# Kernel tuning notes

Hardware: AMD Instinct MI355X
Metric: run time of the kernel (lower is better)

## Reference

```python
import jax, jax.numpy as jnp
import numpy as np

LN_EPS = 1e-5      # torch nn.LayerNorm default
NORM_EPS = 1e-12   # torch F.normalize default


def _layer_norm(x, gamma, beta):
    mu = jnp.mean(x, axis=-1, keepdims=True)
    var = jnp.mean((x - mu) ** 2, axis=-1, keepdims=True)
    return (x - mu) * jax.lax.rsqrt(var + LN_EPS) * gamma + beta


def _l2_normalize_rows(w):
    n = jnp.sqrt(jnp.sum(w * w, axis=1, keepdims=True))
    return w / jnp.maximum(n, NORM_EPS)


def setup_inputs() -> dict:
    key = jax.random.key(0)
    B, D = 32768, 512
    ks = jax.random.split(key, 4)
    return {
        "stimulus": jax.random.normal(ks[0], (B, D), dtype=jnp.float32),
        "prev_activation": jax.random.normal(ks[1], (B, D), dtype=jnp.float32),
        "W": jax.random.normal(ks[2], (D, D), dtype=jnp.float32),
        "Wr": jax.random.normal(ks[3], (D, D), dtype=jnp.float32),
        "alpha": jnp.full((D,), 0.1, dtype=jnp.float32),
        "decay": jnp.full((D,), 0.01, dtype=jnp.float32),
        "ln_act_gamma": jnp.ones((D,), dtype=jnp.float32),
        "ln_act_beta": jnp.zeros((D,), dtype=jnp.float32),
        "ln_rec_gamma": jnp.ones((D,), dtype=jnp.float32),
        "ln_rec_beta": jnp.zeros((D,), dtype=jnp.float32),
    }


def reference(stimulus, prev_activation, W, Wr, alpha, decay,
              ln_act_gamma, ln_act_beta, ln_rec_gamma, ln_rec_beta):
    # recurrent path
    rec_out = prev_activation @ Wr                      # [B, D]
    rec_norm = _layer_norm(rec_out, ln_rec_gamma, ln_rec_beta)
    # stimulus path
    stim_out = stimulus @ W                             # [B, D]
    final = jax.nn.relu(stim_out + rec_norm)
    final = _layer_norm(final, ln_act_gamma, ln_act_beta)

    # Hebbian weight update (detached in the original module)
    heb_upd = jnp.einsum('bi,bj->ij', stimulus, stim_out) * alpha[None, :]
    rec_upd = jnp.einsum('bi,bj->ij', prev_activation, rec_out) * alpha[None, :]
    # diag(decay) @ W is a row-wise broadcast scale
    new_W = _l2_normalize_rows(W + heb_upd - decay[:, None] * W)
    new_Wr = _l2_normalize_rows(Wr + rec_upd - decay[:, None] * Wr)

    return final, new_W, new_Wr
```

## Files before the change

### kernel.cpp

```cpp
#include <hip/hip_runtime.h>
#include <stdint.h>

typedef unsigned int u32;
typedef unsigned short u16;
typedef float  f32x4 __attribute__((ext_vector_type(4)));
typedef u32    u32x4 __attribute__((ext_vector_type(4)));
typedef __bf16 bf16x8 __attribute__((ext_vector_type(8)));

static __device__ __forceinline__ u16 f2bf(float f){
  u32 u = __builtin_bit_cast(u32, f);
  return (u16)((u + 0x7FFFu + ((u >> 16) & 1u)) >> 16);
}

static __device__ __forceinline__ void async16(const void* g, void* l){
  __builtin_amdgcn_global_load_lds((const __attribute__((address_space(1))) u32*)g,
                                   (__attribute__((address_space(3))) u32*)l, 16, 0, 0);
}

static __device__ __forceinline__ float wave_sum(float v){
#pragma unroll
  for (int o = 32; o > 0; o >>= 1) v += __shfl_xor(v, o, 64);
  return v;
}

static __device__ __forceinline__ void prep_tcvt(int sid, const float* __restrict__ W,
                                                 const float* __restrict__ Wr,
                                                 u16* __restrict__ Wt, u16* __restrict__ Wrt,
                                                 u16* lt){
  const int tix = sid & 7, tiy = (sid >> 3) & 7, tiz = sid >> 6;
  const float* __restrict__ src = tiz ? Wr : W;
  u16* __restrict__ dst = tiz ? Wrt : Wt;
  const int c0 = tix * 64, r0 = tiy * 64;
  const int tid = threadIdx.x;
  const int rr = tid >> 4, c4 = tid & 15;
#pragma unroll
  for (int p = 0; p < 4; ++p){
    int r = rr + p*16;
    f32x4 f = *(const f32x4*)(src + (size_t)(r0 + r)*512 + c0 + c4*4);
#pragma unroll
    for (int e = 0; e < 4; ++e) lt[(c4*4 + e)*72 + r] = f2bf(f[e]);
  }
  __syncthreads();
  const int c = tid >> 2, bg = tid & 3;
  const u32x4* lp = (const u32x4*)(lt + c*72 + bg*16);
  u32x4 w0 = lp[0], w1 = lp[1];
  u16* drow = dst + (size_t)(c0 + c)*512 + r0 + bg*16;
  *(u32x4*)drow = w0;
  *(u32x4*)(drow + 8) = w1;
}

__global__ __launch_bounds__(256) void k_prep2(const float* __restrict__ S, const float* __restrict__ P,
                                               const float* __restrict__ W, const float* __restrict__ Wr,
                                               u16* __restrict__ SN, u16* __restrict__ PN,
                                               u16* __restrict__ Wt, u16* __restrict__ Wrt){
  __shared__ u16 lt[64*72];
  const int id = blockIdx.x;
  if (id < 2048){
    const int mat = id >> 10, sub = id & 1023;
    const float* __restrict__ src = mat ? P : S;
    u16* __restrict__ dst = mat ? PN : SN;
    const size_t o0 = ((size_t)sub*256 + threadIdx.x) * 8;
#pragma unroll
    for (int j = 0; j < 8; ++j){
      size_t o = o0 + (size_t)j*2097152;
      f32x4 a = *(const f32x4*)(src + o);
      f32x4 b = *(const f32x4*)(src + o + 4);
      u32x4 w;
      w[0] = (u32)f2bf(a[0]) | ((u32)f2bf(a[1]) << 16);
      w[1] = (u32)f2bf(a[2]) | ((u32)f2bf(a[3]) << 16);
      w[2] = (u32)f2bf(b[0]) | ((u32)f2bf(b[1]) << 16);
      w[3] = (u32)f2bf(b[2]) | ((u32)f2bf(b[3]) << 16);
      *(u32x4*)(dst + o) = w;
    }
  } else {
    prep_tcvt(id - 2048, W, Wr, Wt, Wrt, lt);
  }
}

__global__ __launch_bounds__(512) void k_gemm_fwd(const u16* __restrict__ SN, const u16* __restrict__ PN,
                                                  const u16* __restrict__ Wt, const u16* __restrict__ Wrt,
                                                  u16* __restrict__ SO, u16* __restrict__ RO,
                                                  u16* __restrict__ SOT, u16* __restrict__ ROT){
  __shared__ char smem[67584];
  u16* sA = (u16*)smem;
  u16* sB = (u16*)(smem + 32768);
  const int tid = threadIdx.x;
  const int lane = tid & 63, wid = tid >> 6;
  const int wm = wid >> 1, wn = wid & 1;
  const int l15 = lane & 15, q = lane >> 4;
  const int id = blockIdx.x;
  const int c8 = id & 7, g = id >> 3;
  const int sel = g >> 6, h = g & 63;
  const int yb = c8*16 + (h >> 2), xb = h & 3;
  const int m0 = yb * 256, n0 = xb * 128;
  const u16* __restrict__ A  = sel ? PN  : SN;
  const u16* __restrict__ Bt = sel ? Wrt : Wt;
  u16* __restrict__ Cn = sel ? RO  : SO;
  u16* __restrict__ Ct = sel ? ROT : SOT;

  f32x4 acc[4][4];
  const f32x4 vzero = {0.f, 0.f, 0.f, 0.f};
#pragma unroll
  for (int a = 0; a < 4; ++a)
#pragma unroll
    for (int b = 0; b < 4; ++b) acc[a][b] = vzero;

#pragma unroll 1
  for (int kt = 0; kt < 8; ++kt){
    const int k0 = kt*64;
#pragma unroll
    for (int it = 0; it < 4; ++it){
      int gg0 = it*512 + tid;
      int r = gg0 >> 3, gp = gg0 & 7, gsw = gp ^ (r & 7);
      async16(A + (size_t)(m0 + r)*512 + k0 + gsw*8, (char*)sA + (size_t)gg0*16);
    }
#pragma unroll
    for (int it = 0; it < 2; ++it){
      int gg0 = it*512 + tid;
      int r = gg0 >> 3, gp = gg0 & 7, gsw = gp ^ (r & 7);
      async16(Bt + (size_t)(n0 + r)*512 + k0 + gsw*8, (char*)sB + (size_t)gg0*16);
    }
    __syncthreads();
#pragma unroll
    for (int kk = 0; kk < 2; ++kk){
      bf16x8 af[4], bfv[4];
#pragma unroll
      for (int mt = 0; mt < 4; ++mt){
        int r = wm*64 + mt*16 + l15;
        int gsw = (kk*4 + q) ^ (r & 7);
        af[mt] = *(const bf16x8*)(sA + (size_t)(r*8 + gsw)*8);
      }
#pragma unroll
      for (int nt = 0; nt < 4; ++nt){
        int r = wn*64 + nt*16 + l15;
        int gsw = (kk*4 + q) ^ (r & 7);
        bfv[nt] = *(const bf16x8*)(sB + (size_t)(r*8 + gsw)*8);
      }
#pragma unroll
      for (int mt = 0; mt < 4; ++mt)
#pragma unroll
        for (int nt = 0; nt < 4; ++nt)
          acc[mt][nt] = __builtin_amdgcn_mfma_f32_16x16x32_bf16(af[mt], bfv[nt], acc[mt][nt], 0, 0, 0);
    }
    __syncthreads();
  }

  u16* lt = (u16*)smem;
#pragma unroll
  for (int mt = 0; mt < 4; ++mt)
#pragma unroll
    for (int nt = 0; nt < 4; ++nt){
      f32x4 v = acc[mt][nt];
      u16 b0 = f2bf(v[0]), b1 = f2bf(v[1]), b2 = f2bf(v[2]), b3 = f2bf(v[3]);
      int n = wn*64 + nt*16 + l15;
      int mb = wm*64 + mt*16 + q*4;
      u16* cn = Cn + (size_t)(m0 + mb)*512 + n0 + n;
      cn[0] = b0; cn[512] = b1; cn[1024] = b2; cn[1536] = b3;
      *(u32*)(lt + n*264 + mb)     = (u32)b0 | ((u32)b1 << 16);
      *(u32*)(lt + n*264 + mb + 2) = (u32)b2 | ((u32)b3 << 16);
    }
  __syncthreads();
#pragma unroll
  for (int p = 0; p < 8; ++p){
    int gg0 = p*512 + tid;
    int n = gg0 >> 5, mg = gg0 & 31;
    u32x4 w = *(const u32x4*)(lt + n*264 + mg*8);
    *(u32x4*)(Ct + (size_t)(n0 + n)*32768 + m0 + mg*8) = w;
  }
}

__global__ __launch_bounds__(512) void k_gemm_upd(const u16* __restrict__ A0, const u16* __restrict__ B0,
                                                  const u16* __restrict__ A1, const u16* __restrict__ B1,
                                                  float* __restrict__ part){
  __shared__ char smem[67584];
  char* sAn = smem;
  u32*  sAt = (u32*)(smem + 16384);
  u16*  sB  = (u16*)(smem + 34816);
  const int tid = threadIdx.x;
  const int lane = tid & 63, wid = tid >> 6;
  const int wm = wid >> 2, wn = wid & 3;
  const int l15 = lane & 15, q = lane >> 4;
  const int id = blockIdx.x;
  const int c8 = id & 7, g = id >> 3;
  const int zz = c8*8 + (g >> 3);
  const int xy = g & 7;
  const int mat = zz >> 5, sp = zz & 31;
  const int yb = xy & 3, xb = xy >> 2;
  const u16* __restrict__ A = mat ? A1 : A0;
  const u16* __restrict__ B = mat ? B1 : B0;
  const int m0 = yb * 128, n0 = xb * 256;
  const int kb = sp * 1024;
  const int base_c = tid >> 5, pr = tid & 31;
  const int ce = (base_c + pr) & 15;

  f32x4 acc[4][4];
  const f32x4 vzero = {0.f, 0.f, 0.f, 0.f};
#pragma unroll
  for (int a = 0; a < 4; ++a)
#pragma unroll
    for (int b = 0; b < 4; ++b) acc[a][b] = vzero;

#pragma unroll 1
  for (int kt = 0; kt < 16; ++kt){
    const int k0 = kb + kt*64;
#pragma unroll
    for (int it = 0; it < 2; ++it){
      int gg0 = it*512 + tid;
      int r = gg0 >> 4, gp = gg0 & 15;
      async16(A + (size_t)(k0 + r)*512 + m0 + gp*8, sAn + (size_t)gg0*16);
    }
#pragma unroll
    for (int it = 0; it < 4; ++it){
      int gg0 = it*512 + tid;
      int r = gg0 >> 3, gp = gg0 & 7, gsw = gp ^ (r & 7);
      async16(B + (size_t)(n0 + r)*32768 + k0 + gsw*8, (char*)sB + (size_t)gg0*16);
    }
    __syncthreads();
    {
      u32x4 r0 = *(const u32x4*)(sAn + (size_t)(2*pr)*256 + ce*16);
      u32x4 r1 = *(const u32x4*)(sAn + (size_t)(2*pr)*256 + 256 + ce*16);
#pragma unroll
      for (int e = 0; e < 4; ++e){
        u32 lo = r0[e], hi = r1[e];
        sAt[(ce*8 + 2*e    )*36 + pr] = (lo & 0xFFFFu) | (hi << 16);
        sAt[(ce*8 + 2*e + 1)*36 + pr] = (lo >> 16) | (hi & 0xFFFF0000u);
      }
    }
    __syncthreads();
#pragma unroll
    for (int kk = 0; kk < 2; ++kk){
      bf16x8 af[4], bfv[4];
#pragma unroll
      for (int mt = 0; mt < 4; ++mt){
        int r = wm*64 + mt*16 + l15;
        af[mt] = *(const bf16x8*)(sAt + (size_t)r*36 + kk*16 + q*4);
      }
#pragma unroll
      for (int nt = 0; nt < 4; ++nt){
        int r = wn*64 + nt*16 + l15;
        int gsw = (kk*4 + q) ^ (r & 7);
        bfv[nt] = *(const bf16x8*)(sB + (size_t)(r*8 + gsw)*8);
      }
#pragma unroll
      for (int mt = 0; mt < 4; ++mt)
#pragma unroll
        for (int nt = 0; nt < 4; ++nt)
          acc[mt][nt] = __builtin_amdgcn_mfma_f32_16x16x32_bf16(af[mt], bfv[nt], acc[mt][nt], 0, 0, 0);
    }
    __syncthreads();
  }

  float* dst = part + (size_t)(mat*32 + sp)*262144;
#pragma unroll
  for (int mt = 0; mt < 4; ++mt)
#pragma unroll
    for (int nt = 0; nt < 4; ++nt){
      f32x4 v = acc[mt][nt];
      int n = wn*64 + nt*16 + l15;
      int mb = wm*64 + mt*16 + q*4;
      float* d = dst + (size_t)(m0 + mb)*512 + n0 + n;
      d[0] = v[0]; d[512] = v[1]; d[1024] = v[2]; d[1536] = v[3];
    }
}

__global__ __launch_bounds__(256) void k_ln(const u16* __restrict__ SO, const u16* __restrict__ RO,
                                            const float* __restrict__ ga, const float* __restrict__ ba,
                                            const float* __restrict__ gr, const float* __restrict__ br,
                                            float* __restrict__ out){
  const int wid = threadIdx.x >> 6, lane = threadIdx.x & 63;
  const size_t b = (size_t)blockIdx.x*4 + wid;
  const int c = lane*8;
  float x[8], t[8];
  {
    u32x4 u = *(const u32x4*)(RO + b*512 + c);
#pragma unroll
    for (int i = 0; i < 4; ++i){
      u32 w = u[i];
      x[2*i]   = __uint_as_float(w << 16);
      x[2*i+1] = __uint_as_float(w & 0xFFFF0000u);
    }
  }
  float s = 0.f, ss = 0.f;
#pragma unroll
  for (int e = 0; e < 8; ++e){ s += x[e]; ss += x[e]*x[e]; }
  s = wave_sum(s); ss = wave_sum(ss);
  float mu = s*(1.f/512.f);
  float var = fmaxf(ss*(1.f/512.f) - mu*mu, 0.f);
  float rs = rsqrtf(var + 1e-5f);
  f32x4 g0 = *(const f32x4*)(gr + c), g1 = *(const f32x4*)(gr + c + 4);
  f32x4 h0 = *(const f32x4*)(br + c), h1 = *(const f32x4*)(br + c + 4);
  {
    u32x4 u = *(const u32x4*)(SO + b*512 + c);
    float so[8];
#pragma unroll
    for (int i = 0; i < 4; ++i){
      u32 w = u[i];
      so[2*i]   = __uint_as_float(w << 16);
      so[2*i+1] = __uint_as_float(w & 0xFFFF0000u);
    }
#pragma unroll
    for (int e = 0; e < 4; ++e) t[e]   = fmaxf(so[e]   + (x[e]  -mu)*rs*g0[e] + h0[e], 0.f);
#pragma unroll
    for (int e = 0; e < 4; ++e) t[4+e] = fmaxf(so[4+e] + (x[4+e]-mu)*rs*g1[e] + h1[e], 0.f);
  }
  float s2 = 0.f, ss2 = 0.f;
#pragma unroll
  for (int e = 0; e < 8; ++e){ s2 += t[e]; ss2 += t[e]*t[e]; }
  s2 = wave_sum(s2); ss2 = wave_sum(ss2);
  float mu2 = s2*(1.f/512.f);
  float var2 = fmaxf(ss2*(1.f/512.f) - mu2*mu2, 0.f);
  float rs2 = rsqrtf(var2 + 1e-5f);
  f32x4 G0 = *(const f32x4*)(ga + c), G1 = *(const f32x4*)(ga + c + 4);
  f32x4 H0 = *(const f32x4*)(ba + c), H1 = *(const f32x4*)(ba + c + 4);
  f32x4 o0, o1;
#pragma unroll
  for (int e = 0; e < 4; ++e){
    o0[e] = (t[e]   - mu2)*rs2*G0[e] + H0[e];
    o1[e] = (t[4+e] - mu2)*rs2*G1[e] + H1[e];
  }
  *(f32x4*)(out + b*512 + c)     = o0;
  *(f32x4*)(out + b*512 + c + 4) = o1;
}

__global__ __launch_bounds__(256) void k_finalize(const float* __restrict__ W0, const float* __restrict__ W1,
                                                  const float* __restrict__ part,
                                                  const float* __restrict__ alpha, const float* __restrict__ decay,
                                                  float* __restrict__ out){
  const int i = blockIdx.x, mat = blockIdx.y;
  const int t = threadIdx.x;
  const float* Wm = mat ? W1 : W0;
  const float* pb = part + (size_t)mat*32*262144 + (size_t)i*512;
  const float dc = decay[i];
  float v[2], ssq = 0.f;
#pragma unroll
  for (int h = 0; h < 2; ++h){
    int j = t + h*256;
    float acc = 0.f;
#pragma unroll
    for (int sp = 0; sp < 32; ++sp) acc += pb[(size_t)sp*262144 + j];
    float val = Wm[(size_t)i*512 + j]*(1.f - dc) + alpha[j]*acc;
    v[h] = val; ssq += val*val;
  }
  float wsum = wave_sum(ssq);
  __shared__ float red[4];
  const int lane = t & 63, wid = t >> 6;
  if (lane == 0) red[wid] = wsum;
  __syncthreads();
  float tot = red[0] + red[1] + red[2] + red[3];
  float rn = 1.f / fmaxf(sqrtf(tot), 1e-12f);
  out[(size_t)mat*262144 + (size_t)i*512 + t]       = v[0]*rn;
  out[(size_t)mat*262144 + (size_t)i*512 + t + 256] = v[1]*rn;
}

extern "C" void kernel_launch(void* const* d_in, const int* in_sizes, int n_in,
                              void* d_out, int out_size, void* d_ws, size_t ws_size,
                              hipStream_t stream) {
  const float* S  = (const float*)d_in[0];
  const float* P  = (const float*)d_in[1];
  const float* W  = (const float*)d_in[2];
  const float* Wr = (const float*)d_in[3];
  const float* alpha = (const float*)d_in[4];
  const float* decay = (const float*)d_in[5];
  const float* ga = (const float*)d_in[6];
  const float* ba = (const float*)d_in[7];
  const float* gr = (const float*)d_in[8];
  const float* br = (const float*)d_in[9];
  float* out = (float*)d_out;

  char* ws = (char*)d_ws;
  u16* SN  = (u16*)(ws);
  u16* PN  = (u16*)(ws + 33554432);
  u16* SOT = (u16*)(ws + 67108864);
  u16* ROT = (u16*)(ws + 100663296);
  u16* SO  = (u16*)(ws + 134217728);
  u16* RO  = (u16*)(ws + 167772160);
  u16* Wt  = (u16*)(ws + 201326592);
  u16* Wrt = (u16*)(ws + 201850880);
  float* part = (float*)(ws + 134217728);

  k_prep2<<<dim3(2176), dim3(256), 0, stream>>>(S, P, W, Wr, SN, PN, Wt, Wrt);
  k_gemm_fwd<<<dim3(1024), dim3(512), 0, stream>>>(SN, PN, Wt, Wrt, SO, RO, SOT, ROT);
  k_ln<<<dim3(8192), dim3(256), 0, stream>>>(SO, RO, ga, ba, gr, br, out);
  k_gemm_upd<<<dim3(512), dim3(512), 0, stream>>>(SN, SOT, PN, ROT, part);
  k_finalize<<<dim3(512, 2), dim3(256), 0, stream>>>(W, Wr, part, alpha, decay, out + 16777216);
}
```

Baseline: 325.5 us.

## Fuse forward GEMMs with both LayerNorms into one full-row kernel

Replaces the separate forward GEMM and LayerNorm kernels with one kernel in which each block computes full 512-column rows for both the stimulus and recurrent GEMMs, keeps the stimulus result packed in registers, and applies both LayerNorms in-register using a cross-wave shared-memory reduction. This drops the SO/RO row-major bf16 intermediates and the extra LN pass over them, still writing only the transposed copies needed by the update GEMM. The prep kernel is also reshaped to one chunk per block. The catch is that only 256 blocks are launched, each carrying a large register accumulator, so occupancy and parallelism drop.

```diff
diff --git a/kernel.cpp b/kernel.cpp
--- a/kernel.cpp
+++ b/kernel.cpp
@@ -23,107 +23,75 @@
   return v;
 }
 
-static __device__ __forceinline__ void prep_tcvt(int sid, const float* __restrict__ W,
-                                                 const float* __restrict__ Wr,
-                                                 u16* __restrict__ Wt, u16* __restrict__ Wrt,
-                                                 u16* lt){
-  const int tix = sid & 7, tiy = (sid >> 3) & 7, tiz = sid >> 6;
-  const float* __restrict__ src = tiz ? Wr : W;
-  u16* __restrict__ dst = tiz ? Wrt : Wt;
-  const int c0 = tix * 64, r0 = tiy * 64;
-  const int tid = threadIdx.x;
-  const int rr = tid >> 4, c4 = tid & 15;
-#pragma unroll
-  for (int p = 0; p < 4; ++p){
-    int r = rr + p*16;
-    f32x4 f = *(const f32x4*)(src + (size_t)(r0 + r)*512 + c0 + c4*4);
-#pragma unroll
-    for (int e = 0; e < 4; ++e) lt[(c4*4 + e)*72 + r] = f2bf(f[e]);
-  }
-  __syncthreads();
-  const int c = tid >> 2, bg = tid & 3;
-  const u32x4* lp = (const u32x4*)(lt + c*72 + bg*16);
-  u32x4 w0 = lp[0], w1 = lp[1];
-  u16* drow = dst + (size_t)(c0 + c)*512 + r0 + bg*16;
-  *(u32x4*)drow = w0;
-  *(u32x4*)(drow + 8) = w1;
-}
-
-__global__ __launch_bounds__(256) void k_prep2(const float* __restrict__ S, const float* __restrict__ P,
-                                               const float* __restrict__ W, const float* __restrict__ Wr,
-                                               u16* __restrict__ SN, u16* __restrict__ PN,
-                                               u16* __restrict__ Wt, u16* __restrict__ Wrt){
+__global__ __launch_bounds__(256) void k_prep(const float* __restrict__ S, const float* __restrict__ P,
+                                              const float* __restrict__ W, const float* __restrict__ Wr,
+                                              u16* __restrict__ SN, u16* __restrict__ PN,
+                                              u16* __restrict__ Wt, u16* __restrict__ Wrt){
   __shared__ u16 lt[64*72];
   const int id = blockIdx.x;
-  if (id < 2048){
-    const int mat = id >> 10, sub = id & 1023;
-    const float* __restrict__ src = mat ? P : S;
-    u16* __restrict__ dst = mat ? PN : SN;
-    const size_t o0 = ((size_t)sub*256 + threadIdx.x) * 8;
-#pragma unroll
-    for (int j = 0; j < 8; ++j){
-      size_t o = o0 + (size_t)j*2097152;
-      f32x4 a = *(const f32x4*)(src + o);
-      f32x4 b = *(const f32x4*)(src + o + 4);
-      u32x4 w;
-      w[0] = (u32)f2bf(a[0]) | ((u32)f2bf(a[1]) << 16);
-      w[1] = (u32)f2bf(a[2]) | ((u32)f2bf(a[3]) << 16);
-      w[2] = (u32)f2bf(b[0]) | ((u32)f2bf(b[1]) << 16);
-      w[3] = (u32)f2bf(b[2]) | ((u32)f2bf(b[3]) << 16);
-      *(u32x4*)(dst + o) = w;
-    }
+  if (id < 16384){
+    const int y = id >> 13, x = id & 8191;
+    const float* __restrict__ src = y ? P : S;
+    u16* __restrict__ dst = y ? PN : SN;
+    size_t i = ((size_t)x*256 + threadIdx.x) * 8;
+    f32x4 a = *(const f32x4*)(src + i);
+    f32x4 b = *(const f32x4*)(src + i + 4);
+    u32x4 w;
+    w[0] = (u32)f2bf(a[0]) | ((u32)f2bf(a[1]) << 16);
+    w[1] = (u32)f2bf(a[2]) | ((u32)f2bf(a[3]) << 16);
+    w[2] = (u32)f2bf(b[0]) | ((u32)f2bf(b[1]) << 16);
+    w[3] = (u32)f2bf(b[2]) | ((u32)f2bf(b[3]) << 16);
+    *(u32x4*)(dst + i) = w;
   } else {
-    prep_tcvt(id - 2048, W, Wr, Wt, Wrt, lt);
-  }
-}
-
-__global__ __launch_bounds__(512) void k_gemm_fwd(const u16* __restrict__ SN, const u16* __restrict__ PN,
-                                                  const u16* __restrict__ Wt, const u16* __restrict__ Wrt,
-                                                  u16* __restrict__ SO, u16* __restrict__ RO,
-                                                  u16* __restrict__ SOT, u16* __restrict__ ROT){
-  __shared__ char smem[67584];
+    const int sid = id - 16384;
+    const int tix = sid & 7, tiy = (sid >> 3) & 7, tiz = sid >> 6;
+    const float* __restrict__ src = tiz ? Wr : W;
+    u16* __restrict__ dst = tiz ? Wrt : Wt;
+    const int c0 = tix * 64, r0 = tiy * 64;
+    const int tid = threadIdx.x;
+    const int rr = tid >> 4, c4 = tid & 15;
+#pragma unroll
+    for (int p = 0; p < 4; ++p){
+      int r = rr + p*16;
+      f32x4 f = *(const f32x4*)(src + (size_t)(r0 + r)*512 + c0 + c4*4);
+#pragma unroll
+      for (int e = 0; e < 4; ++e) lt[(c4*4 + e)*72 + r] = f2bf(f[e]);
+    }
+    __syncthreads();
+    const int c = tid >> 2, bg = tid & 3;
+    const u32x4* lp = (const u32x4*)(lt + c*72 + bg*16);
+    u32x4 w0 = lp[0], w1 = lp[1];
+    u16* drow = dst + (size_t)(c0 + c)*512 + r0 + bg*16;
+    *(u32x4*)drow = w0;
+    *(u32x4*)(drow + 8) = w1;
+  }
+}
+
+
+static __device__ __forceinline__ void gemm_phase(const u16* __restrict__ A, const u16* __restrict__ Bt,
+                                                  f32x4 (&acc)[4][8], char* smem,
+                                                  int tid, int wm, int wn, int l15, int q, int m0){
   u16* sA = (u16*)smem;
-  u16* sB = (u16*)(smem + 32768);
-  const int tid = threadIdx.x;
-  const int lane = tid & 63, wid = tid >> 6;
-  const int wm = wid >> 1, wn = wid & 1;
-  const int l15 = lane & 15, q = lane >> 4;
-  const int id = blockIdx.x;
-  const int c8 = id & 7, g = id >> 3;
-  const int sel = g >> 6, h = g & 63;
-  const int yb = c8*16 + (h >> 2), xb = h & 3;
-  const int m0 = yb * 256, n0 = xb * 128;
-  const u16* __restrict__ A  = sel ? PN  : SN;
-  const u16* __restrict__ Bt = sel ? Wrt : Wt;
-  u16* __restrict__ Cn = sel ? RO  : SO;
-  u16* __restrict__ Ct = sel ? ROT : SOT;
-
-  f32x4 acc[4][4];
-  const f32x4 vzero = {0.f, 0.f, 0.f, 0.f};
-#pragma unroll
-  for (int a = 0; a < 4; ++a)
-#pragma unroll
-    for (int b = 0; b < 4; ++b) acc[a][b] = vzero;
-
+  u16* sB = (u16*)(smem + 16384);
 #pragma unroll 1
   for (int kt = 0; kt < 8; ++kt){
     const int k0 = kt*64;
 #pragma unroll
-    for (int it = 0; it < 4; ++it){
-      int gg0 = it*512 + tid;
-      int r = gg0 >> 3, gp = gg0 & 7, gsw = gp ^ (r & 7);
-      async16(A + (size_t)(m0 + r)*512 + k0 + gsw*8, (char*)sA + (size_t)gg0*16);
-    }
-#pragma unroll
     for (int it = 0; it < 2; ++it){
-      int gg0 = it*512 + tid;
-      int r = gg0 >> 3, gp = gg0 & 7, gsw = gp ^ (r & 7);
-      async16(Bt + (size_t)(n0 + r)*512 + k0 + gsw*8, (char*)sB + (size_t)gg0*16);
+      int gg = it*512 + tid;
+      int r = gg >> 3, gp = gg & 7, gsw = gp ^ (r & 7);
+      async16(A + (size_t)(m0 + r)*512 + k0 + gsw*8, (char*)sA + (size_t)gg*16);
+    }
+#pragma unroll
+    for (int it = 0; it < 8; ++it){
+      int gg = it*512 + tid;
+      int r = gg >> 3, gp = gg & 7, gsw = gp ^ (r & 7);
+      async16(Bt + (size_t)r*512 + k0 + gsw*8, (char*)sB + (size_t)gg*16);
     }
     __syncthreads();
 #pragma unroll
     for (int kk = 0; kk < 2; ++kk){
-      bf16x8 af[4], bfv[4];
+      bf16x8 af[4], bfv[8];
 #pragma unroll
       for (int mt = 0; mt < 4; ++mt){
         int r = wm*64 + mt*16 + l15;
@@ -131,42 +99,204 @@
         af[mt] = *(const bf16x8*)(sA + (size_t)(r*8 + gsw)*8);
       }
 #pragma unroll
-      for (int nt = 0; nt < 4; ++nt){
-        int r = wn*64 + nt*16 + l15;
+      for (int nt = 0; nt < 8; ++nt){
+        int r = wn*128 + nt*16 + l15;
         int gsw = (kk*4 + q) ^ (r & 7);
         bfv[nt] = *(const bf16x8*)(sB + (size_t)(r*8 + gsw)*8);
       }
 #pragma unroll
       for (int mt = 0; mt < 4; ++mt)
 #pragma unroll
-        for (int nt = 0; nt < 4; ++nt)
+        for (int nt = 0; nt < 8; ++nt)
           acc[mt][nt] = __builtin_amdgcn_mfma_f32_16x16x32_bf16(af[mt], bfv[nt], acc[mt][nt], 0, 0, 0);
     }
     __syncthreads();
   }
-
+}
+
+static __device__ __forceinline__ void store_T(const f32x4 (&acc)[4][8], u16* __restrict__ Ct, char* smem,
+                                               int tid, int wm, int wn, int l15, int q, int m0){
   u16* lt = (u16*)smem;
+#pragma unroll 1
+  for (int jc = 0; jc < 4; ++jc){
+    if (wn == jc){
+#pragma unroll
+      for (int mt = 0; mt < 4; ++mt)
+#pragma unroll
+        for (int nt = 0; nt < 8; ++nt){
+          f32x4 v = acc[mt][nt];
+          int jl = nt*16 + l15;
+          int bl = wm*64 + mt*16 + q*4;
+          *(u32*)(lt + jl*264 + bl)     = (u32)f2bf(v[0]) | ((u32)f2bf(v[1]) << 16);
+          *(u32*)(lt + jl*264 + bl + 2) = (u32)f2bf(v[2]) | ((u32)f2bf(v[3]) << 16);
+        }
+    }
+    __syncthreads();
+#pragma unroll
+    for (int p = 0; p < 4; ++p){
+      int gg = p*512 + tid;
+      int j = gg >> 4, mg = gg & 15;
+      u32x4 w = *(const u32x4*)(lt + j*264 + mg*8);
+      *(u32x4*)(Ct + (size_t)(jc*128 + j)*32768 + m0 + mg*8) = w;
+    }
+    __syncthreads();
+  }
+}
+
+__global__ __launch_bounds__(512) void k_fused(const u16* __restrict__ SN, const u16* __restrict__ PN,
+                                               const u16* __restrict__ Wt, const u16* __restrict__ Wrt,
+                                               const float* __restrict__ ga, const float* __restrict__ ba,
+                                               const float* __restrict__ gr, const float* __restrict__ br,
+                                               u16* __restrict__ SOT, u16* __restrict__ ROT,
+                                               float* __restrict__ out){
+  __shared__ char smem[81920];
+  float* red = (float*)(smem + 69632);
+  const int tid = threadIdx.x;
+  const int lane = tid & 63, wid = tid >> 6;
+  const int wm = wid >> 2, wn = wid & 3;
+  const int l15 = lane & 15, q = lane >> 4;
+  const int id = blockIdx.x;
+  const int m0 = ((id & 7)*32 + (id >> 3)) * 128;
+
+  f32x4 acc[4][8];
+  const f32x4 vzero = {0.f, 0.f, 0.f, 0.f};
+
+#pragma unroll
+  for (int a = 0; a < 4; ++a)
+#pragma unroll
+    for (int b = 0; b < 8; ++b) acc[a][b] = vzero;
+  gemm_phase(SN, Wt, acc, smem, tid, wm, wn, l15, q, m0);
+  store_T(acc, SOT, smem, tid, wm, wn, l15, q, m0);
+
+  u32 ps[4][8][2];
 #pragma unroll
   for (int mt = 0; mt < 4; ++mt)
 #pragma unroll
-    for (int nt = 0; nt < 4; ++nt){
+    for (int nt = 0; nt < 8; ++nt){
       f32x4 v = acc[mt][nt];
-      u16 b0 = f2bf(v[0]), b1 = f2bf(v[1]), b2 = f2bf(v[2]), b3 = f2bf(v[3]);
-      int n = wn*64 + nt*16 + l15;
-      int mb = wm*64 + mt*16 + q*4;
-      u16* cn = Cn + (size_t)(m0 + mb)*512 + n0 + n;
-      cn[0] = b0; cn[512] = b1; cn[1024] = b2; cn[1536] = b3;
-      *(u32*)(lt + n*264 + mb)     = (u32)b0 | ((u32)b1 << 16);
-      *(u32*)(lt + n*264 + mb + 2) = (u32)b2 | ((u32)b3 << 16);
-    }
-  __syncthreads();
-#pragma unroll
-  for (int p = 0; p < 8; ++p){
-    int gg0 = p*512 + tid;
-    int n = gg0 >> 5, mg = gg0 & 31;
-    u32x4 w = *(const u32x4*)(lt + n*264 + mg*8);
-    *(u32x4*)(Ct + (size_t)(n0 + n)*32768 + m0 + mg*8) = w;
-  }
+      ps[mt][nt][0] = (u32)f2bf(v[0]) | ((u32)f2bf(v[1]) << 16);
+      ps[mt][nt][1] = (u32)f2bf(v[2]) | ((u32)f2bf(v[3]) << 16);
+    }
+
+#pragma unroll
+  for (int a = 0; a < 4; ++a)
+#pragma unroll
+    for (int b = 0; b < 8; ++b) acc[a][b] = vzero;
+  gemm_phase(PN, Wrt, acc, smem, tid, wm, wn, l15, q, m0);
+  store_T(acc, ROT, smem, tid, wm, wn, l15, q, m0);
+
+  float mu[4][4], irs[4][4];
+
+  {
+    float sb[4][4], qb[4][4];
+#pragma unroll
+    for (int mt = 0; mt < 4; ++mt)
+#pragma unroll
+      for (int e = 0; e < 4; ++e){
+        float s = 0.f, ss = 0.f;
+#pragma unroll
+        for (int nt = 0; nt < 8; ++nt){ float v = acc[mt][nt][e]; s += v; ss += v*v; }
+#pragma unroll
+        for (int o = 1; o < 16; o <<= 1){ s += __shfl_xor(s, o, 64); ss += __shfl_xor(ss, o, 64); }
+        sb[mt][e] = s; qb[mt][e] = ss;
+      }
+    if (l15 == 0){
+#pragma unroll
+      for (int mt = 0; mt < 4; ++mt)
+#pragma unroll
+        for (int e = 0; e < 4; ++e){
+          int row = wm*64 + mt*16 + q*4 + e;
+          red[row*8 + wn*2]     = sb[mt][e];
+          red[row*8 + wn*2 + 1] = qb[mt][e];
+        }
+    }
+    __syncthreads();
+#pragma unroll
+    for (int mt = 0; mt < 4; ++mt)
+#pragma unroll
+      for (int e = 0; e < 4; ++e){
+        int row = wm*64 + mt*16 + q*4 + e;
+        float S = red[row*8] + red[row*8+2] + red[row*8+4] + red[row*8+6];
+        float Q = red[row*8+1] + red[row*8+3] + red[row*8+5] + red[row*8+7];
+        float m_ = S * (1.f/512.f);
+        float v_ = fmaxf(Q * (1.f/512.f) - m_*m_, 0.f);
+        mu[mt][e] = m_;
+        irs[mt][e] = rsqrtf(v_ + 1e-5f);
+      }
+    __syncthreads();
+  }
+
+  float grv[8], brv[8];
+#pragma unroll
+  for (int nt = 0; nt < 8; ++nt){
+    int col = wn*128 + nt*16 + l15;
+    grv[nt] = gr[col]; brv[nt] = br[col];
+  }
+#pragma unroll
+  for (int mt = 0; mt < 4; ++mt)
+#pragma unroll
+    for (int nt = 0; nt < 8; ++nt)
+#pragma unroll
+      for (int e = 0; e < 4; ++e){
+        u32 w = ps[mt][nt][e >> 1];
+        float stim = __uint_as_float((e & 1) ? (w & 0xFFFF0000u) : (w << 16));
+        float v = stim + (acc[mt][nt][e] - mu[mt][e]) * irs[mt][e] * grv[nt] + brv[nt];
+        acc[mt][nt][e] = fmaxf(v, 0.f);
+      }
+
+  {
+    float sb[4][4], qb[4][4];
+#pragma unroll
+    for (int mt = 0; mt < 4; ++mt)
+#pragma unroll
+      for (int e = 0; e < 4; ++e){
+        float s = 0.f, ss = 0.f;
+#pragma unroll
+        for (int nt = 0; nt < 8; ++nt){ float v = acc[mt][nt][e]; s += v; ss += v*v; }
+#pragma unroll
+        for (int o = 1; o < 16; o <<= 1){ s += __shfl_xor(s, o, 64); ss += __shfl_xor(ss, o, 64); }
+        sb[mt][e] = s; qb[mt][e] = ss;
+      }
+    if (l15 == 0){
+#pragma unroll
+      for (int mt = 0; mt < 4; ++mt)
+#pragma unroll
+        for (int e = 0; e < 4; ++e){
+          int row = wm*64 + mt*16 + q*4 + e;
+          red[row*8 + wn*2]     = sb[mt][e];
+          red[row*8 + wn*2 + 1] = qb[mt][e];
+        }
+    }
+    __syncthreads();
+#pragma unroll
+    for (int mt = 0; mt < 4; ++mt)
+#pragma unroll
+      for (int e = 0; e < 4; ++e){
+        int row = wm*64 + mt*16 + q*4 + e;
+        float S = red[row*8] + red[row*8+2] + red[row*8+4] + red[row*8+6];
+        float Q = red[row*8+1] + red[row*8+3] + red[row*8+5] + red[row*8+7];
+        float m_ = S * (1.f/512.f);
+        float v_ = fmaxf(Q * (1.f/512.f) - m_*m_, 0.f);
+        mu[mt][e] = m_;
+        irs[mt][e] = rsqrtf(v_ + 1e-5f);
+      }
+  }
+
+#pragma unroll
+  for (int nt = 0; nt < 8; ++nt){
+    int col = wn*128 + nt*16 + l15;
+    grv[nt] = ga[col]; brv[nt] = ba[col];
+  }
+#pragma unroll
+  for (int mt = 0; mt < 4; ++mt)
+#pragma unroll
+    for (int e = 0; e < 4; ++e){
+      float m_ = mu[mt][e], r_ = irs[mt][e];
+      size_t rowoff = (size_t)(m0 + wm*64 + mt*16 + q*4 + e) * 512 + wn*128 + l15;
+#pragma unroll
+      for (int nt = 0; nt < 8; ++nt)
+        out[rowoff + nt*16] = (acc[mt][nt][e] - m_) * r_ * grv[nt] + brv[nt];
+    }
 }
 
 __global__ __launch_bounds__(512) void k_gemm_upd(const u16* __restrict__ A0, const u16* __restrict__ B0,
@@ -263,65 +393,6 @@
     }
 }
 
-__global__ __launch_bounds__(256) void k_ln(const u16* __restrict__ SO, const u16* __restrict__ RO,
-                                            const float* __restrict__ ga, const float* __restrict__ ba,
-                                            const float* __restrict__ gr, const float* __restrict__ br,
-                                            float* __restrict__ out){
-  const int wid = threadIdx.x >> 6, lane = threadIdx.x & 63;
-  const size_t b = (size_t)blockIdx.x*4 + wid;
-  const int c = lane*8;
-  float x[8], t[8];
-  {
-    u32x4 u = *(const u32x4*)(RO + b*512 + c);
-#pragma unroll
-    for (int i = 0; i < 4; ++i){
-      u32 w = u[i];
-      x[2*i]   = __uint_as_float(w << 16);
-      x[2*i+1] = __uint_as_float(w & 0xFFFF0000u);
-    }
-  }
-  float s = 0.f, ss = 0.f;
-#pragma unroll
-  for (int e = 0; e < 8; ++e){ s += x[e]; ss += x[e]*x[e]; }
-  s = wave_sum(s); ss = wave_sum(ss);
-  float mu = s*(1.f/512.f);
-  float var = fmaxf(ss*(1.f/512.f) - mu*mu, 0.f);
-  float rs = rsqrtf(var + 1e-5f);
-  f32x4 g0 = *(const f32x4*)(gr + c), g1 = *(const f32x4*)(gr + c + 4);
-  f32x4 h0 = *(const f32x4*)(br + c), h1 = *(const f32x4*)(br + c + 4);
-  {
-    u32x4 u = *(const u32x4*)(SO + b*512 + c);
-    float so[8];
-#pragma unroll
-    for (int i = 0; i < 4; ++i){
-      u32 w = u[i];
-      so[2*i]   = __uint_as_float(w << 16);
-      so[2*i+1] = __uint_as_float(w & 0xFFFF0000u);
-    }
-#pragma unroll
-    for (int e = 0; e < 4; ++e) t[e]   = fmaxf(so[e]   + (x[e]  -mu)*rs*g0[e] + h0[e], 0.f);
-#pragma unroll
-    for (int e = 0; e < 4; ++e) t[4+e] = fmaxf(so[4+e] + (x[4+e]-mu)*rs*g1[e] + h1[e], 0.f);
-  }
-  float s2 = 0.f, ss2 = 0.f;
-#pragma unroll
-  for (int e = 0; e < 8; ++e){ s2 += t[e]; ss2 += t[e]*t[e]; }
-  s2 = wave_sum(s2); ss2 = wave_sum(ss2);
-  float mu2 = s2*(1.f/512.f);
-  float var2 = fmaxf(ss2*(1.f/512.f) - mu2*mu2, 0.f);
-  float rs2 = rsqrtf(var2 + 1e-5f);
-  f32x4 G0 = *(const f32x4*)(ga + c), G1 = *(const f32x4*)(ga + c + 4);
-  f32x4 H0 = *(const f32x4*)(ba + c), H1 = *(const f32x4*)(ba + c + 4);
-  f32x4 o0, o1;
-#pragma unroll
-  for (int e = 0; e < 4; ++e){
-    o0[e] = (t[e]   - mu2)*rs2*G0[e] + H0[e];
-    o1[e] = (t[4+e] - mu2)*rs2*G1[e] + H1[e];
-  }
-  *(f32x4*)(out + b*512 + c)     = o0;
-  *(f32x4*)(out + b*512 + c + 4) = o1;
-}
-
 __global__ __launch_bounds__(256) void k_finalize(const float* __restrict__ W0, const float* __restrict__ W1,
                                                   const float* __restrict__ part,
                                                   const float* __restrict__ alpha, const float* __restrict__ decay,
@@ -372,15 +443,12 @@
   u16* PN  = (u16*)(ws + 33554432);
   u16* SOT = (u16*)(ws + 67108864);
   u16* ROT = (u16*)(ws + 100663296);
-  u16* SO  = (u16*)(ws + 134217728);
-  u16* RO  = (u16*)(ws + 167772160);
-  u16* Wt  = (u16*)(ws + 201326592);
-  u16* Wrt = (u16*)(ws + 201850880);
-  float* part = (float*)(ws + 134217728);
-
-  k_prep2<<<dim3(2176), dim3(256), 0, stream>>>(S, P, W, Wr, SN, PN, Wt, Wrt);
-  k_gemm_fwd<<<dim3(1024), dim3(512), 0, stream>>>(SN, PN, Wt, Wrt, SO, RO, SOT, ROT);
-  k_ln<<<dim3(8192), dim3(256), 0, stream>>>(SO, RO, ga, ba, gr, br, out);
+  u16* Wt  = (u16*)(ws + 134217728);
+  u16* Wrt = (u16*)(ws + 134742016);
+  float* part = (float*)(ws + 135266304);
+
+  k_prep<<<dim3(16512), dim3(256), 0, stream>>>(S, P, W, Wr, SN, PN, Wt, Wrt);
+  k_fused<<<dim3(256), dim3(512), 0, stream>>>(SN, PN, Wt, Wrt, ga, ba, gr, br, SOT, ROT, out);
   k_gemm_upd<<<dim3(512), dim3(512), 0, stream>>>(SN, SOT, PN, ROT, part);
   k_finalize<<<dim3(512, 2), dim3(256), 0, stream>>>(W, Wr, part, alpha, decay, out + 16777216);
 }
```

After: 370.9 us. 1.14x slower.
